# Kernel optimization log

Measured on AMD Instinct MI355X. Metric: run time of the kernel, lower is better.

Reference implementation:

```python
import jax, jax.numpy as jnp
import numpy as np

N, E = 768, 24576
NODE_DIM, EDGE_DIM, HID = 8, 4, 8
MLP_HID = 4 * HID  # 32


def _mlp(x, params):
    # torch nn.Linear: y = x @ W.T + b; ReLU after every layer except the last
    *hidden, last = params
    for W, b in hidden:
        x = jax.nn.relu(x @ W.T + b)
    W, b = last
    return x @ W.T + b


def _init_mlp(key, dims):
    params = []
    for din, dout in zip(dims[:-1], dims[1:]):
        key, k1, k2 = jax.random.split(key, 3)
        lim = 1.0 / np.sqrt(din)
        W = jax.random.uniform(k1, (dout, din), minval=-lim, maxval=lim, dtype=jnp.float32)
        b = jax.random.uniform(k2, (dout,), minval=-lim, maxval=lim, dtype=jnp.float32)
        params.append((W, b))
    return params


def setup_inputs() -> dict:
    key = jax.random.key(0)
    k_mtr, k_feat, k_ei, k_ea, k_emlp, k_omlp = jax.random.split(key, 6)
    inp = {
        "mtr": jax.random.normal(k_mtr, (N, N, HID), dtype=jnp.float32),
        "feat": jax.random.normal(k_feat, (N, NODE_DIM), dtype=jnp.float32),
        "edge_index": jax.random.randint(k_ei, (2, E), 0, N, dtype=jnp.int64),
        "edge_attr": jax.random.normal(k_ea, (E, EDGE_DIM), dtype=jnp.float32),
    }
    edge_in_dim = EDGE_DIM + 2 * NODE_DIM              # 20
    out_in_dim = 2 * HID + 2 * NODE_DIM + 1            # 33
    eparams = _init_mlp(k_emlp, [edge_in_dim, MLP_HID, MLP_HID, MLP_HID, HID * HID])
    oparams = _init_mlp(k_omlp, [out_in_dim, MLP_HID, MLP_HID, MLP_HID, HID])
    for i, (W, b) in enumerate(eparams):
        inp[f"e_w{i}"], inp[f"e_b{i}"] = W, b
    for i, (W, b) in enumerate(oparams):
        inp[f"o_w{i}"], inp[f"o_b{i}"] = W, b
    return inp


def reference(mtr, feat, edge_index, edge_attr,
              e_w0, e_b0, e_w1, e_b1, e_w2, e_b2, e_w3, e_b3,
              o_w0, o_b0, o_w1, o_b1, o_w2, o_b2, o_w3, o_b3):
    n, h = mtr.shape[0], mtr.shape[2]
    eparams = [(e_w0, e_b0), (e_w1, e_b1), (e_w2, e_b2), (e_w3, e_b3)]
    oparams = [(o_w0, o_b0), (o_w1, o_b1), (o_w2, o_b2), (o_w3, o_b3)]
    src, dst = edge_index[0], edge_index[1]
    # edge MLP on [E, edge_dim + 2*node_dim]
    edge_in = jnp.concatenate([edge_attr, feat[src], feat[dst]], axis=-1)
    evals = _mlp(edge_in, eparams).reshape(-1, h, h)  # [E, h, h]
    # scatter into dense [n, n, h, h] adjacency tensor (zeros for non-edges)
    fmtr = jnp.zeros((n, n, h, h), dtype=mtr.dtype).at[src, dst].set(evals)
    # walk contraction over (j, c)
    mtr1 = jnp.einsum('ijc,jkct->ikt', mtr, fmtr) / h  # [n, n, h]
    eye = jnp.eye(n, dtype=mtr.dtype)[:, :, None]                       # [n, n, 1]
    feat_j = jnp.broadcast_to(feat[None, :, :], (n, n, feat.shape[-1]))  # row-broadcast
    feat_i = jnp.broadcast_to(feat[:, None, :], (n, n, feat.shape[-1]))  # col-broadcast
    cat = jnp.concatenate(
        [mtr1, jnp.transpose(mtr1, (1, 0, 2)), feat_j, feat_i, eye], axis=-1)  # [n, n, 33]
    return mtr + _mlp(cat, oparams)
```

## Files before the change

kernel.cpp:

```cpp
#include <hip/hip_runtime.h>

#define N 768
#define E 24576
#define NPAD_SLOTS (E + 3 * 768)
#define NGROUPS (NPAD_SLOTS / 4)
#define MLIST_SLOTS (NPAD_SLOTS + 16)

typedef __attribute__((ext_vector_type(8))) short bf16x8;
typedef __attribute__((ext_vector_type(4))) float f32x4;

__device__ __forceinline__ unsigned pk2(float lo, float hi) {
  unsigned r;
  asm("v_cvt_pk_bf16_f32 %0, %1, %2" : "=v"(r) : "v"(lo), "v"(hi));
  return r;
}

union FragU {
  unsigned u[4];
  bf16x8 s;
};

__device__ __forceinline__ bf16x8 pack_frag(float4 a, float4 b) {
  FragU f;
  f.u[0] = pk2(a.x, a.y);
  f.u[1] = pk2(a.z, a.w);
  f.u[2] = pk2(b.x, b.y);
  f.u[3] = pk2(b.z, b.w);
  return f.s;
}

__device__ __forceinline__ bf16x8 relu_pack(f32x4 d1, f32x4 d2) {
  FragU f;
  f.u[0] = pk2(fmaxf(d1[0], 0.f), fmaxf(d1[1], 0.f));
  f.u[1] = pk2(fmaxf(d1[2], 0.f), fmaxf(d1[3], 0.f));
  f.u[2] = pk2(fmaxf(d2[0], 0.f), fmaxf(d2[1], 0.f));
  f.u[3] = pk2(fmaxf(d2[2], 0.f), fmaxf(d2[3], 0.f));
  return f.s;
}

__device__ __forceinline__ f32x4 ld4(const float* p) {
  float4 v = *(const float4*)p;
  f32x4 r;
  r[0] = v.x; r[1] = v.y; r[2] = v.z; r[3] = v.w;
  return r;
}

__global__ __launch_bounds__(256) void init_ws(int4* __restrict__ winner4,
                                               float4* __restrict__ Mlist4,
                                               int* __restrict__ jlist,
                                               int* __restrict__ deg,
                                               int* __restrict__ curs) {
  const int t = blockIdx.x * 256 + threadIdx.x;
  Mlist4[t] = make_float4(0.f, 0.f, 0.f, 0.f);
  if (t < 147456) winner4[t] = make_int4(-1, -1, -1, -1);
  if (t < NPAD_SLOTS) jlist[t] = 0;
  if (t < 1024) { deg[t] = 0; curs[t] = 0; }
}

__global__ __launch_bounds__(256) void transpose_mtr_bf(
    const float* __restrict__ mtr, uint4* __restrict__ mtrT) {
  __shared__ float lds[16][16 * 8 + 4];
  const int r = threadIdx.x >> 4;
  const int c = threadIdx.x & 15;
  const size_t i0 = (size_t)blockIdx.y * 16;
  const size_t j0 = (size_t)blockIdx.x * 16;

  const float4* src = (const float4*)(mtr + ((i0 + r) * N + (j0 + c)) * 8);
  float4 a = src[0], b = src[1];
  *(float4*)&lds[r][c * 8 + 0] = a;
  *(float4*)&lds[r][c * 8 + 4] = b;
  __syncthreads();
  float4 ta = *(float4*)&lds[c][r * 8 + 0];
  float4 tb = *(float4*)&lds[c][r * 8 + 4];
  uint4 o;
  o.x = pk2(ta.x, ta.y); o.y = pk2(ta.z, ta.w);
  o.z = pk2(tb.x, tb.y); o.w = pk2(tb.z, tb.w);
  mtrT[(j0 + r) * N + (i0 + c)] = o;
}

__global__ __launch_bounds__(256) void edge_prep(
    const int* __restrict__ ei, int* __restrict__ winner,
    int* __restrict__ deg) {
  const int e = blockIdx.x * 256 + threadIdx.x;
  if (e >= E) return;
  const int s = ei[e];
  const int d = ei[E + e];
  atomicMax(&winner[(size_t)s * N + d], e);
  atomicAdd(&deg[d], 1);
}

__global__ void scan_offs(const int* __restrict__ deg, int* __restrict__ offs) {
  const int lane = threadIdx.x;
  int v[12];
  int s = 0;
#pragma unroll
  for (int z = 0; z < 12; ++z) {
    v[z] = (deg[lane * 12 + z] + 3) & ~3;
    s += v[z];
  }
  int inc = s;
#pragma unroll
  for (int d = 1; d < 64; d <<= 1) {
    int t = __shfl_up(inc, d, 64);
    if (lane >= d) inc += t;
  }
  int run = inc - s;
#pragma unroll
  for (int z = 0; z < 12; ++z) {
    run += v[z];
    offs[lane * 12 + z + 1] = run;
  }
  if (lane == 0) offs[0] = 0;
}

__global__ __launch_bounds__(256) void scatter_pos(
    const int* __restrict__ ei, const int* __restrict__ winner,
    const int* __restrict__ offs, int* __restrict__ curs,
    int* __restrict__ jlist, int* __restrict__ epos) {
  const int e = blockIdx.x * 256 + threadIdx.x;
  if (e >= E) return;
  const int s = ei[e];
  const int d = ei[E + e];
  if (winner[(size_t)s * N + d] != e) { epos[e] = -1; return; }
  const int pos = offs[d] + atomicAdd(&curs[d], 1);
  jlist[pos] = s;
  epos[e] = pos;
}

__global__ __launch_bounds__(64) void edge_mlp_mfma(
    const float* __restrict__ feat, const int* __restrict__ ei,
    const float* __restrict__ ea, const int* __restrict__ epos,
    const float* __restrict__ w0, const float* __restrict__ b0,
    const float* __restrict__ w1, const float* __restrict__ b1,
    const float* __restrict__ w2, const float* __restrict__ b2,
    const float* __restrict__ w3, const float* __restrict__ b3,
    float* __restrict__ Mlist) {
  const int col = threadIdx.x & 15;
  const int hi = (threadIdx.x >> 4) & 3;
  const int e = blockIdx.x * 16 + col;

  const float4 z4 = make_float4(0.f, 0.f, 0.f, 0.f);

  const int s = ei[e];
  const int d = ei[E + e];
  const int pos = epos[e];
  const float* pa = (hi == 0) ? (ea + (size_t)e * 4)
                  : (hi == 1) ? (feat + (size_t)s * 8)
                  : (hi == 2) ? (feat + (size_t)s * 8 + 4)
                              : (feat + (size_t)d * 8);
  float4 va = *(const float4*)pa;
  float4 vb = (hi == 0) ? *(const float4*)(feat + (size_t)d * 8 + 4) : z4;
  bf16x8 bfr = pack_frag(va, vb);

  bf16x8 a0lo, a0hi, a1lo, a1hi, a2lo, a2hi, a3f[4];
  {
    const float* p = w0 + col * 20;
    float4 xa = *(const float4*)(p + hi * 4);
    float4 xb = (hi == 0) ? *(const float4*)(p + 16) : z4;
    a0lo = pack_frag(xa, xb);
    const float* q = w0 + (col + 16) * 20;
    float4 ya = *(const float4*)(q + hi * 4);
    float4 yb = (hi == 0) ? *(const float4*)(q + 16) : z4;
    a0hi = pack_frag(ya, yb);
  }
  a1lo = pack_frag(*(const float4*)(w1 + col * 32 + hi * 4),
                   *(const float4*)(w1 + col * 32 + 16 + hi * 4));
  a1hi = pack_frag(*(const float4*)(w1 + (col + 16) * 32 + hi * 4),
                   *(const float4*)(w1 + (col + 16) * 32 + 16 + hi * 4));
  a2lo = pack_frag(*(const float4*)(w2 + col * 32 + hi * 4),
                   *(const float4*)(w2 + col * 32 + 16 + hi * 4));
  a2hi = pack_frag(*(const float4*)(w2 + (col + 16) * 32 + hi * 4),
                   *(const float4*)(w2 + (col + 16) * 32 + 16 + hi * 4));
#pragma unroll
  for (int q = 0; q < 4; ++q) {
    const float* p = w3 + (size_t)(q * 16 + col) * 32;
    a3f[q] = pack_frag(*(const float4*)(p + hi * 4),
                       *(const float4*)(p + 16 + hi * 4));
  }

  f32x4 d1 = ld4(b0 + hi * 4), d2 = ld4(b0 + 16 + hi * 4);
  d1 = __builtin_amdgcn_mfma_f32_16x16x32_bf16(a0lo, bfr, d1, 0, 0, 0);
  d2 = __builtin_amdgcn_mfma_f32_16x16x32_bf16(a0hi, bfr, d2, 0, 0, 0);
  bfr = relu_pack(d1, d2);

  d1 = ld4(b1 + hi * 4); d2 = ld4(b1 + 16 + hi * 4);
  d1 = __builtin_amdgcn_mfma_f32_16x16x32_bf16(a1lo, bfr, d1, 0, 0, 0);
  d2 = __builtin_amdgcn_mfma_f32_16x16x32_bf16(a1hi, bfr, d2, 0, 0, 0);
  bfr = relu_pack(d1, d2);

  d1 = ld4(b2 + hi * 4); d2 = ld4(b2 + 16 + hi * 4);
  d1 = __builtin_amdgcn_mfma_f32_16x16x32_bf16(a2lo, bfr, d1, 0, 0, 0);
  d2 = __builtin_amdgcn_mfma_f32_16x16x32_bf16(a2hi, bfr, d2, 0, 0, 0);
  bfr = relu_pack(d1, d2);

#pragma unroll
  for (int q = 0; q < 4; ++q) {
    f32x4 d3 = ld4(b3 + q * 16 + hi * 4);
    d3 = __builtin_amdgcn_mfma_f32_16x16x32_bf16(a3f[q], bfr, d3, 0, 0, 0);
    if (pos >= 0) {
      *(float4*)(Mlist + (size_t)pos * 64 + q * 16 + hi * 4) =
          make_float4(d3[0], d3[1], d3[2], d3[3]);
    }
  }
}

__global__ __launch_bounds__(256) void repack_mfrag(
    const float* __restrict__ Mlist, short* __restrict__ Mfrag) {
  __shared__ float L[4][256];
  const int w = threadIdx.x >> 6;
  const int lane = threadIdx.x & 63;
  const int gid = blockIdx.x * 4 + w;

  *(float4*)&L[w][lane * 4] =
      *(const float4*)(Mlist + (size_t)gid * 256 + lane * 4);
  __syncthreads();

  const int col = lane & 15;
  const int hi = lane >> 4;
  const int g0 = hi >> 1;
  const int c0 = (hi & 1) * 4;

  float a[4] = {0.f, 0.f, 0.f, 0.f}, b[4] = {0.f, 0.f, 0.f, 0.f};
  if (col < 8) {
#pragma unroll
    for (int j = 0; j < 4; ++j) {
      a[j] = L[w][g0 * 64 + (c0 + j) * 8 + col];
      b[j] = L[w][(2 + g0) * 64 + (c0 + j) * 8 + col];
    }
  }
  FragU f;
  f.u[0] = pk2(a[0], a[1]);
  f.u[1] = pk2(a[2], a[3]);
  f.u[2] = pk2(b[0], b[1]);
  f.u[3] = pk2(b[2], b[3]);
  *(bf16x8*)(Mfrag + (size_t)gid * 512 + lane * 8) = f.s;
}

__global__ __launch_bounds__(256) void contract6(
    const short* __restrict__ mtrT, const short* __restrict__ Mfrag,
    const int* __restrict__ jlist, const int* __restrict__ offs,
    const int* __restrict__ wcnt, float* __restrict__ WT) {
  __shared__ float sD[4][4][16][9];

  const int bid = blockIdx.x;
  const int g = (bid & 7) * 288 + (bid >> 3);
  const int ig = g / 768;
  const int k = g % 768;
  const int w = threadIdx.x >> 6;
  const int lane = threadIdx.x & 63;
  const int col = lane & 15;
  const int hi = lane >> 4;
  const int ibase = ig * 256 + w * 64;

  const int base = offs[k];
  const int cnt = wcnt[k];
  const int ngr = (cnt + 3) >> 2;

  f32x4 acc0 = {0.f, 0.f, 0.f, 0.f}, acc1 = {0.f, 0.f, 0.f, 0.f};
  f32x4 acc2 = {0.f, 0.f, 0.f, 0.f}, acc3 = {0.f, 0.f, 0.f, 0.f};

  const size_t lane_off = ((size_t)(ibase + col)) * 8 + (hi & 1) * 4;

#pragma unroll 1
  for (int gg = 0; gg < ngr; ++gg) {
    const int4 js = *(const int4*)(jlist + base + gg * 4);
    const int ja = (hi & 2) ? js.y : js.x;
    const int jb = (hi & 2) ? js.w : js.z;

    bf16x8 bfr = *(const bf16x8*)(
        Mfrag + ((size_t)(base >> 2) + gg) * 512 + lane * 8);

    const short* pa = mtrT + (size_t)ja * (N * 8) + lane_off;
    const short* pb = mtrT + (size_t)jb * (N * 8) + lane_off;

#define TILE(ACC, T)                                                     \
  do {                                                                   \
    uint2 ua = *(const uint2*)(pa + (T) * (16 * 8));                     \
    uint2 ub = *(const uint2*)(pb + (T) * (16 * 8));                     \
    FragU af;                                                            \
    af.u[0] = ua.x; af.u[1] = ua.y; af.u[2] = ub.x; af.u[3] = ub.y;      \
    ACC = __builtin_amdgcn_mfma_f32_16x16x32_bf16(af.s, bfr, ACC, 0, 0, 0); \
  } while (0)

    TILE(acc0, 0);
    TILE(acc1, 1);
    TILE(acc2, 2);
    TILE(acc3, 3);
#undef TILE
  }

  if (col < 8) {
#pragma unroll
    for (int r = 0; r < 4; ++r) {
      sD[w][0][hi * 4 + r][col] = acc0[r] * 0.125f;
      sD[w][1][hi * 4 + r][col] = acc1[r] * 0.125f;
      sD[w][2][hi * 4 + r][col] = acc2[r] * 0.125f;
      sD[w][3][hi * 4 + r][col] = acc3[r] * 0.125f;
    }
  }
  __syncthreads();
  if (lane < 16) {
#pragma unroll
    for (int t = 0; t < 4; ++t) {
      const float* row = &sD[w][t][lane][0];
      float* dst = WT + ((size_t)k * N + ibase + t * 16 + lane) * 8;
      *(float4*)(dst + 0) = make_float4(row[0], row[1], row[2], row[3]);
      *(float4*)(dst + 4) = make_float4(row[4], row[5], row[6], row[7]);
    }
  }
}

__global__ __launch_bounds__(256, 2) void out_mlp_mfma(
    const float* __restrict__ mtr, const float* __restrict__ WT,
    const float* __restrict__ feat,
    const float* __restrict__ w0, const float* __restrict__ b0,
    const float* __restrict__ w1, const float* __restrict__ b1,
    const float* __restrict__ w2, const float* __restrict__ b2,
    const float* __restrict__ w3, const float* __restrict__ b3,
    float* __restrict__ out) {
  const int i = blockIdx.y;
  const int k0 = blockIdx.x * 256;
  const int w = threadIdx.x >> 6;
  const int col = threadIdx.x & 15;
  const int hi = (threadIdx.x >> 4) & 3;

  bf16x8 a0lo, a0hi, a1lo, a1hi, a2lo, a2hi, a3;
  {
    const float* p = w0 + col * 33;
    float4 xa = make_float4(p[hi * 4], p[hi * 4 + 1], p[hi * 4 + 2], p[hi * 4 + 3]);
    float4 xb = make_float4(p[16 + hi * 4], p[16 + hi * 4 + 1],
                            p[16 + hi * 4 + 2], p[16 + hi * 4 + 3]);
    a0lo = pack_frag(xa, xb);
    const float* q = w0 + (col + 16) * 33;
    float4 ya = make_float4(q[hi * 4], q[hi * 4 + 1], q[hi * 4 + 2], q[hi * 4 + 3]);
    float4 yb = make_float4(q[16 + hi * 4], q[16 + hi * 4 + 1],
                            q[16 + hi * 4 + 2], q[16 + hi * 4 + 3]);
    a0hi = pack_frag(ya, yb);
  }
  a1lo = pack_frag(*(const float4*)(w1 + col * 32 + hi * 4),
                   *(const float4*)(w1 + col * 32 + 16 + hi * 4));
  a1hi = pack_frag(*(const float4*)(w1 + (col + 16) * 32 + hi * 4),
                   *(const float4*)(w1 + (col + 16) * 32 + 16 + hi * 4));
  a2lo = pack_frag(*(const float4*)(w2 + col * 32 + hi * 4),
                   *(const float4*)(w2 + col * 32 + 16 + hi * 4));
  a2hi = pack_frag(*(const float4*)(w2 + (col + 16) * 32 + hi * 4),
                   *(const float4*)(w2 + (col + 16) * 32 + 16 + hi * 4));
  if (col < 8) {
    a3 = pack_frag(*(const float4*)(w3 + col * 32 + hi * 4),
                   *(const float4*)(w3 + col * 32 + 16 + hi * 4));
  } else {
    FragU z; z.u[0] = z.u[1] = z.u[2] = z.u[3] = 0; a3 = z.s;
  }

  const f32x4 c1a = ld4(b0 + hi * 4), c1b = ld4(b0 + 16 + hi * 4);
  const f32x4 c2a = ld4(b1 + hi * 4), c2b = ld4(b1 + 16 + hi * 4);
  const f32x4 c3a = ld4(b2 + hi * 4), c3b = ld4(b2 + 16 + hi * 4);
  f32x4 c4;
  if (hi < 2) c4 = ld4(b3 + hi * 4);
  else { c4[0] = c4[1] = c4[2] = c4[3] = 0.f; }

  float dg1[4], dg2[4];
#pragma unroll
  for (int r = 0; r < 4; ++r) {
    dg1[r] = w0[(hi * 4 + r) * 33 + 32];
    dg2[r] = w0[(16 + hi * 4 + r) * 33 + 32];
  }

#pragma unroll 1
  for (int g = 0; g < 4; ++g) {
    const int krow = k0 + w * 64 + g * 16 + col;

    const float* pA = (hi < 2) ? (WT + ((size_t)krow * N + i) * 8 + (hi & 1) * 4)
                               : (WT + ((size_t)i * N + krow) * 8 + (hi & 1) * 4);
    const float* pB = (hi < 2) ? (feat + (size_t)krow * 8 + (hi & 1) * 4)
                               : (feat + (size_t)i * 8 + (hi & 1) * 4);
    bf16x8 bfr = pack_frag(*(const float4*)pA, *(const float4*)pB);

    f32x4 d1 = c1a, d2 = c1b;
    d1 = __builtin_amdgcn_mfma_f32_16x16x32_bf16(a0lo, bfr, d1, 0, 0, 0);
    d2 = __builtin_amdgcn_mfma_f32_16x16x32_bf16(a0hi, bfr, d2, 0, 0, 0);
    const float eye = (krow == i) ? 1.f : 0.f;
#pragma unroll
    for (int r = 0; r < 4; ++r) {
      d1[r] = fmaf(eye, dg1[r], d1[r]);
      d2[r] = fmaf(eye, dg2[r], d2[r]);
    }
    bfr = relu_pack(d1, d2);

    d1 = c2a; d2 = c2b;
    d1 = __builtin_amdgcn_mfma_f32_16x16x32_bf16(a1lo, bfr, d1, 0, 0, 0);
    d2 = __builtin_amdgcn_mfma_f32_16x16x32_bf16(a1hi, bfr, d2, 0, 0, 0);
    bfr = relu_pack(d1, d2);

    d1 = c3a; d2 = c3b;
    d1 = __builtin_amdgcn_mfma_f32_16x16x32_bf16(a2lo, bfr, d1, 0, 0, 0);
    d2 = __builtin_amdgcn_mfma_f32_16x16x32_bf16(a2hi, bfr, d2, 0, 0, 0);
    bfr = relu_pack(d1, d2);

    f32x4 d3 = c4;
    d3 = __builtin_amdgcn_mfma_f32_16x16x32_bf16(a3, bfr, d3, 0, 0, 0);

    if (hi < 2) {
      const size_t idx = ((size_t)i * N + krow) * 8 + hi * 4;
      float4 m = *(const float4*)(mtr + idx);
      *(float4*)(out + idx) =
          make_float4(m.x + d3[0], m.y + d3[1], m.z + d3[2], m.w + d3[3]);
    }
  }
}

extern "C" void kernel_launch(void* const* d_in, const int* in_sizes, int n_in,
                              void* d_out, int out_size, void* d_ws,
                              size_t ws_size, hipStream_t stream) {
  const float* mtr  = (const float*)d_in[0];
  const float* feat = (const float*)d_in[1];
  const int*   ei   = (const int*)d_in[2];
  const float* ea   = (const float*)d_in[3];
  const float* ew0 = (const float*)d_in[4];
  const float* eb0 = (const float*)d_in[5];
  const float* ew1 = (const float*)d_in[6];
  const float* eb1 = (const float*)d_in[7];
  const float* ew2 = (const float*)d_in[8];
  const float* eb2 = (const float*)d_in[9];
  const float* ew3 = (const float*)d_in[10];
  const float* eb3 = (const float*)d_in[11];
  const float* ow0 = (const float*)d_in[12];
  const float* ob0 = (const float*)d_in[13];
  const float* ow1 = (const float*)d_in[14];
  const float* ob1 = (const float*)d_in[15];
  const float* ow2 = (const float*)d_in[16];
  const float* ob2 = (const float*)d_in[17];
  const float* ow3 = (const float*)d_in[18];
  const float* ob3 = (const float*)d_in[19];
  float* out = (float*)d_out;

  char* ws = (char*)d_ws;
  float* Mlist = (float*)ws; ws += (size_t)MLIST_SLOTS * 64 * 4;
  short* Mfrag = (short*)ws; ws += (size_t)NGROUPS * 512 * 2;
  short* mtrT  = (short*)ws; ws += (size_t)N * N * 8 * 2;
  float* WT    = (float*)ws; ws += (size_t)N * N * 8 * 4;
  int* winner  = (int*)ws;   ws += (size_t)N * N * 4;
  int* deg     = (int*)ws;   ws += 1024 * 4;
  int* offs    = (int*)ws;   ws += 1024 * 4;
  int* curs    = (int*)ws;   ws += 1024 * 4;
  int* jlist   = (int*)ws;   ws += (size_t)NPAD_SLOTS * 4;
  int* epos    = (int*)ws;   ws += (size_t)E * 4;

  init_ws<<<1681, 256, 0, stream>>>((int4*)winner, (float4*)Mlist, jlist, deg,
                                    curs);
  edge_prep<<<E / 256, 256, 0, stream>>>(ei, winner, deg);
  scan_offs<<<1, 64, 0, stream>>>(deg, offs);
  scatter_pos<<<E / 256, 256, 0, stream>>>(ei, winner, offs, curs, jlist, epos);
  transpose_mtr_bf<<<dim3(48, 48), 256, 0, stream>>>(mtr, (uint4*)mtrT);
  edge_mlp_mfma<<<E / 16, 64, 0, stream>>>(feat, ei, ea, epos, ew0, eb0, ew1,
                                           eb1, ew2, eb2, ew3, eb3, Mlist);
  repack_mfrag<<<NGROUPS / 4, 256, 0, stream>>>(Mlist, Mfrag);
  contract6<<<2304, 256, 0, stream>>>(mtrT, Mfrag, jlist, offs, curs, WT);
  out_mlp_mfma<<<dim3(3, N), 256, 0, stream>>>(mtr, WT, feat, ow0, ob0, ow1,
                                               ob1, ow2, ob2, ow3, ob3, out);
}
```

Measured before the change: 105.6 us.

## Fuse prep kernels, store WT in bf16, and enlarge out-MLP blocks

```diff
diff --git a/kernel.cpp b/kernel.cpp
--- a/kernel.cpp
+++ b/kernel.cpp
@@ -45,105 +45,108 @@
   return r;
 }
 
-__global__ __launch_bounds__(256) void init_ws(int4* __restrict__ winner4,
-                                               float4* __restrict__ Mlist4,
-                                               int* __restrict__ jlist,
-                                               int* __restrict__ deg,
-                                               int* __restrict__ curs) {
-  const int t = blockIdx.x * 256 + threadIdx.x;
-  Mlist4[t] = make_float4(0.f, 0.f, 0.f, 0.f);
-  if (t < 147456) winner4[t] = make_int4(-1, -1, -1, -1);
-  if (t < NPAD_SLOTS) jlist[t] = 0;
-  if (t < 1024) { deg[t] = 0; curs[t] = 0; }
-}
-
-__global__ __launch_bounds__(256) void transpose_mtr_bf(
-    const float* __restrict__ mtr, uint4* __restrict__ mtrT) {
+__global__ __launch_bounds__(256) void prep0(
+    const float* __restrict__ mtr, uint4* __restrict__ mtrT,
+    int4* __restrict__ winner4, float4* __restrict__ Mlist4,
+    int* __restrict__ jlist, int* __restrict__ deg, int* __restrict__ curs,
+    int* __restrict__ done_ctr) {
   __shared__ float lds[16][16 * 8 + 4];
-  const int r = threadIdx.x >> 4;
-  const int c = threadIdx.x & 15;
-  const size_t i0 = (size_t)blockIdx.y * 16;
-  const size_t j0 = (size_t)blockIdx.x * 16;
-
-  const float4* src = (const float4*)(mtr + ((i0 + r) * N + (j0 + c)) * 8);
-  float4 a = src[0], b = src[1];
-  *(float4*)&lds[r][c * 8 + 0] = a;
-  *(float4*)&lds[r][c * 8 + 4] = b;
-  __syncthreads();
-  float4 ta = *(float4*)&lds[c][r * 8 + 0];
-  float4 tb = *(float4*)&lds[c][r * 8 + 4];
-  uint4 o;
-  o.x = pk2(ta.x, ta.y); o.y = pk2(ta.z, ta.w);
-  o.z = pk2(tb.x, tb.y); o.w = pk2(tb.z, tb.w);
-  mtrT[(j0 + r) * N + (i0 + c)] = o;
-}
-
-__global__ __launch_bounds__(256) void edge_prep(
+  if (blockIdx.x < 2304) {
+    const int r = threadIdx.x >> 4;
+    const int c = threadIdx.x & 15;
+    const size_t j0 = (size_t)(blockIdx.x % 48) * 16;
+    const size_t i0 = (size_t)(blockIdx.x / 48) * 16;
+
+    const float4* src = (const float4*)(mtr + ((i0 + r) * N + (j0 + c)) * 8);
+    float4 a = src[0], b = src[1];
+    *(float4*)&lds[r][c * 8 + 0] = a;
+    *(float4*)&lds[r][c * 8 + 4] = b;
+    __syncthreads();
+    float4 ta = *(float4*)&lds[c][r * 8 + 0];
+    float4 tb = *(float4*)&lds[c][r * 8 + 4];
+    uint4 o;
+    o.x = pk2(ta.x, ta.y); o.y = pk2(ta.z, ta.w);
+    o.z = pk2(tb.x, tb.y); o.w = pk2(tb.z, tb.w);
+    mtrT[(j0 + r) * N + (i0 + c)] = o;
+  } else {
+    const int t = (blockIdx.x - 2304) * 256 + threadIdx.x;
+    Mlist4[t] = make_float4(0.f, 0.f, 0.f, 0.f);
+    if (t < 147456) winner4[t] = make_int4(-1, -1, -1, -1);
+    if (t < NPAD_SLOTS) jlist[t] = 0;
+    if (t < 1024) { deg[t] = 0; curs[t] = 0; }
+    if (t == 0) *done_ctr = 0;
+  }
+}
+
+__global__ __launch_bounds__(256) void edge_prep_scan(
     const int* __restrict__ ei, int* __restrict__ winner,
-    int* __restrict__ deg) {
+    int* __restrict__ deg, int* __restrict__ offs,
+    int* __restrict__ done_ctr) {
   const int e = blockIdx.x * 256 + threadIdx.x;
-  if (e >= E) return;
   const int s = ei[e];
   const int d = ei[E + e];
   atomicMax(&winner[(size_t)s * N + d], e);
   atomicAdd(&deg[d], 1);
-}
-
-__global__ void scan_offs(const int* __restrict__ deg, int* __restrict__ offs) {
-  const int lane = threadIdx.x;
-  int v[12];
-  int s = 0;
-#pragma unroll
-  for (int z = 0; z < 12; ++z) {
-    v[z] = (deg[lane * 12 + z] + 3) & ~3;
-    s += v[z];
-  }
-  int inc = s;
-#pragma unroll
-  for (int d = 1; d < 64; d <<= 1) {
-    int t = __shfl_up(inc, d, 64);
-    if (lane >= d) inc += t;
-  }
-  int run = inc - s;
-#pragma unroll
-  for (int z = 0; z < 12; ++z) {
-    run += v[z];
-    offs[lane * 12 + z + 1] = run;
-  }
-  if (lane == 0) offs[0] = 0;
-}
-
-__global__ __launch_bounds__(256) void scatter_pos(
-    const int* __restrict__ ei, const int* __restrict__ winner,
+
+  __threadfence();
+  __syncthreads();
+  __shared__ int ticket;
+  if (threadIdx.x == 0) ticket = atomicAdd(done_ctr, 1);
+  __syncthreads();
+  if (ticket == (E / 256) - 1 && threadIdx.x < 64) {
+    const int lane = threadIdx.x;
+    int v[12];
+    int sum = 0;
+#pragma unroll
+    for (int z = 0; z < 12; ++z) {
+      v[z] = (atomicAdd(&deg[lane * 12 + z], 0) + 3) & ~3;
+      sum += v[z];
+    }
+    int inc = sum;
+#pragma unroll
+    for (int dd = 1; dd < 64; dd <<= 1) {
+      int t = __shfl_up(inc, dd, 64);
+      if (lane >= dd) inc += t;
+    }
+    int run = inc - sum;
+#pragma unroll
+    for (int z = 0; z < 12; ++z) {
+      run += v[z];
+      offs[lane * 12 + z + 1] = run;
+    }
+    if (lane == 0) offs[0] = 0;
+  }
+}
+
+__global__ __launch_bounds__(256) void edge_mlp_mfma(
+    const float* __restrict__ feat, const int* __restrict__ ei,
+    const float* __restrict__ ea, const int* __restrict__ winner,
     const int* __restrict__ offs, int* __restrict__ curs,
-    int* __restrict__ jlist, int* __restrict__ epos) {
-  const int e = blockIdx.x * 256 + threadIdx.x;
-  if (e >= E) return;
-  const int s = ei[e];
-  const int d = ei[E + e];
-  if (winner[(size_t)s * N + d] != e) { epos[e] = -1; return; }
-  const int pos = offs[d] + atomicAdd(&curs[d], 1);
-  jlist[pos] = s;
-  epos[e] = pos;
-}
-
-__global__ __launch_bounds__(64) void edge_mlp_mfma(
-    const float* __restrict__ feat, const int* __restrict__ ei,
-    const float* __restrict__ ea, const int* __restrict__ epos,
+    int* __restrict__ jlist,
     const float* __restrict__ w0, const float* __restrict__ b0,
     const float* __restrict__ w1, const float* __restrict__ b1,
     const float* __restrict__ w2, const float* __restrict__ b2,
     const float* __restrict__ w3, const float* __restrict__ b3,
     float* __restrict__ Mlist) {
-  const int col = threadIdx.x & 15;
-  const int hi = (threadIdx.x >> 4) & 3;
-  const int e = blockIdx.x * 16 + col;
+  const int wv = threadIdx.x >> 6;
+  const int lane = threadIdx.x & 63;
+  const int col = lane & 15;
+  const int hi = lane >> 4;
+  const int e = (blockIdx.x * 4 + wv) * 16 + col;
 
   const float4 z4 = make_float4(0.f, 0.f, 0.f, 0.f);
 
   const int s = ei[e];
   const int d = ei[E + e];
-  const int pos = epos[e];
+  int pos = -1;
+  if (hi == 0) {
+    if (winner[(size_t)s * N + d] == e) {
+      pos = offs[d] + atomicAdd(&curs[d], 1);
+      jlist[pos] = s;
+    }
+  }
+  pos = __shfl(pos, col, 64);
+
   const float* pa = (hi == 0) ? (ea + (size_t)e * 4)
                   : (hi == 1) ? (feat + (size_t)s * 8)
                   : (hi == 2) ? (feat + (size_t)s * 8 + 4)
@@ -236,10 +239,10 @@
   *(bf16x8*)(Mfrag + (size_t)gid * 512 + lane * 8) = f.s;
 }
 
-__global__ __launch_bounds__(256) void contract6(
+__global__ __launch_bounds__(256) void contract7(
     const short* __restrict__ mtrT, const short* __restrict__ Mfrag,
     const int* __restrict__ jlist, const int* __restrict__ offs,
-    const int* __restrict__ wcnt, float* __restrict__ WT) {
+    const int* __restrict__ wcnt, short* __restrict__ WTb) {
   __shared__ float sD[4][4][16][9];
 
   const int bid = blockIdx.x;
@@ -303,23 +306,23 @@
 #pragma unroll
     for (int t = 0; t < 4; ++t) {
       const float* row = &sD[w][t][lane][0];
-      float* dst = WT + ((size_t)k * N + ibase + t * 16 + lane) * 8;
-      *(float4*)(dst + 0) = make_float4(row[0], row[1], row[2], row[3]);
-      *(float4*)(dst + 4) = make_float4(row[4], row[5], row[6], row[7]);
+      uint4 o;
+      o.x = pk2(row[0], row[1]); o.y = pk2(row[2], row[3]);
+      o.z = pk2(row[4], row[5]); o.w = pk2(row[6], row[7]);
+      *(uint4*)(WTb + ((size_t)k * N + ibase + t * 16 + lane) * 8) = o;
     }
   }
 }
 
 __global__ __launch_bounds__(256, 2) void out_mlp_mfma(
-    const float* __restrict__ mtr, const float* __restrict__ WT,
+    const float* __restrict__ mtr, const short* __restrict__ WTb,
     const float* __restrict__ feat,
     const float* __restrict__ w0, const float* __restrict__ b0,
     const float* __restrict__ w1, const float* __restrict__ b1,
     const float* __restrict__ w2, const float* __restrict__ b2,
     const float* __restrict__ w3, const float* __restrict__ b3,
     float* __restrict__ out) {
-  const int i = blockIdx.y;
-  const int k0 = blockIdx.x * 256;
+  const int i = blockIdx.x;
   const int w = threadIdx.x >> 6;
   const int col = threadIdx.x & 15;
   const int hi = (threadIdx.x >> 4) & 3;
@@ -367,14 +370,20 @@
   }
 
 #pragma unroll 1
-  for (int g = 0; g < 4; ++g) {
-    const int krow = k0 + w * 64 + g * 16 + col;
-
-    const float* pA = (hi < 2) ? (WT + ((size_t)krow * N + i) * 8 + (hi & 1) * 4)
-                               : (WT + ((size_t)i * N + krow) * 8 + (hi & 1) * 4);
-    const float* pB = (hi < 2) ? (feat + (size_t)krow * 8 + (hi & 1) * 4)
+  for (int g = 0; g < 12; ++g) {
+    const int krow = w * 192 + g * 16 + col;
+
+    FragU bf;
+    const short* pW = (hi < 2)
+        ? (WTb + ((size_t)krow * N + i) * 8 + (hi & 1) * 4)
+        : (WTb + ((size_t)i * N + krow) * 8 + (hi & 1) * 4);
+    uint2 wv2 = *(const uint2*)pW;
+    const float* pF = (hi < 2) ? (feat + (size_t)krow * 8 + (hi & 1) * 4)
                                : (feat + (size_t)i * 8 + (hi & 1) * 4);
-    bf16x8 bfr = pack_frag(*(const float4*)pA, *(const float4*)pB);
+    float4 fv = *(const float4*)pF;
+    bf.u[0] = wv2.x; bf.u[1] = wv2.y;
+    bf.u[2] = pk2(fv.x, fv.y); bf.u[3] = pk2(fv.z, fv.w);
+    bf16x8 bfr = bf.s;
 
     f32x4 d1 = c1a, d2 = c1b;
     d1 = __builtin_amdgcn_mfma_f32_16x16x32_bf16(a0lo, bfr, d1, 0, 0, 0);
@@ -438,24 +447,23 @@
   float* Mlist = (float*)ws; ws += (size_t)MLIST_SLOTS * 64 * 4;
   short* Mfrag = (short*)ws; ws += (size_t)NGROUPS * 512 * 2;
   short* mtrT  = (short*)ws; ws += (size_t)N * N * 8 * 2;
-  float* WT    = (float*)ws; ws += (size_t)N * N * 8 * 4;
+  short* WTb   = (short*)ws; ws += (size_t)N * N * 8 * 2;
   int* winner  = (int*)ws;   ws += (size_t)N * N * 4;
   int* deg     = (int*)ws;   ws += 1024 * 4;
   int* offs    = (int*)ws;   ws += 1024 * 4;
   int* curs    = (int*)ws;   ws += 1024 * 4;
+  int* done_ctr = (int*)ws;  ws += 256 * 4;
   int* jlist   = (int*)ws;   ws += (size_t)NPAD_SLOTS * 4;
-  int* epos    = (int*)ws;   ws += (size_t)E * 4;
-
-  init_ws<<<1681, 256, 0, stream>>>((int4*)winner, (float4*)Mlist, jlist, deg,
-                                    curs);
-  edge_prep<<<E / 256, 256, 0, stream>>>(ei, winner, deg);
-  scan_offs<<<1, 64, 0, stream>>>(deg, offs);
-  scatter_pos<<<E / 256, 256, 0, stream>>>(ei, winner, offs, curs, jlist, epos);
-  transpose_mtr_bf<<<dim3(48, 48), 256, 0, stream>>>(mtr, (uint4*)mtrT);
-  edge_mlp_mfma<<<E / 16, 64, 0, stream>>>(feat, ei, ea, epos, ew0, eb0, ew1,
-                                           eb1, ew2, eb2, ew3, eb3, Mlist);
+
+  prep0<<<2304 + 1681, 256, 0, stream>>>(mtr, (uint4*)mtrT, (int4*)winner,
+                                         (float4*)Mlist, jlist, deg, curs,
+                                         done_ctr);
+  edge_prep_scan<<<E / 256, 256, 0, stream>>>(ei, winner, deg, offs, done_ctr);
+  edge_mlp_mfma<<<E / 64, 256, 0, stream>>>(feat, ei, ea, winner, offs, curs,
+                                            jlist, ew0, eb0, ew1, eb1, ew2,
+                                            eb2, ew3, eb3, Mlist);
   repack_mfrag<<<NGROUPS / 4, 256, 0, stream>>>(Mlist, Mfrag);
-  contract6<<<2304, 256, 0, stream>>>(mtrT, Mfrag, jlist, offs, curs, WT);
-  out_mlp_mfma<<<dim3(3, N), 256, 0, stream>>>(mtr, WT, feat, ow0, ob0, ow1,
-                                               ob1, ow2, ob2, ow3, ob3, out);
-}
+  contract7<<<2304, 256, 0, stream>>>(mtrT, Mfrag, jlist, offs, curs, WTb);
+  out_mlp_mfma<<<N, 256, 0, stream>>>(mtr, WTb, feat, ow0, ob0, ow1, ob1, ow2,
+                                      ob2, ow3, ob3, out);
+}
```

New measurement: 93.72 us. 1.13x faster.
